# Kernel tuning notes

Measured on AMD Instinct MI355X. Metric: run time of the kernel, lower is better.

The kernel has to match this reference:

```python
import jax, jax.numpy as jnp
import numpy as np

# Model dims (from init_kwargs)
D_MODEL = 1024
D_STATE = 64
D_CONV = 4
EXPAND = 2
HEADDIM = 128
NGROUPS = 1
D_INNER = EXPAND * D_MODEL              # 2048
NHEADS = D_INNER // HEADDIM             # 16
CONV_DIM = D_INNER + 2 * NGROUPS * D_STATE   # 2176
D_IN_PROJ = 2 * D_INNER + 2 * NGROUPS * D_STATE + NHEADS  # 4240
BATCH, SEQLEN = 2, 2048
DT_MIN, DT_MAX, DT_FLOOR = 1e-3, 1e-1, 1e-4
RMS_EPS = 1e-5


def setup_inputs() -> dict:
    key = jax.random.key(0)
    ks = jax.random.split(key, 8)
    u = jax.random.normal(ks[0], (BATCH, SEQLEN, D_MODEL), jnp.float32)
    in_proj_w = jax.random.normal(ks[1], (D_IN_PROJ, D_MODEL), jnp.float32) * 0.02
    conv_w = jax.random.normal(ks[2], (CONV_DIM, 1, D_CONV), jnp.float32) * 0.2
    conv_b = jax.random.normal(ks[3], (CONV_DIM,), jnp.float32) * 0.02
    # dt_bias init: inverse-softplus of dt ~ LogUniform(dt_min, dt_max)
    dt = jnp.exp(jax.random.uniform(ks[4], (NHEADS,)) * (jnp.log(DT_MAX) - jnp.log(DT_MIN)) + jnp.log(DT_MIN))
    dt = jnp.maximum(dt, DT_FLOOR)
    dt_bias = dt + jnp.log(-jnp.expm1(-dt))
    A_log = jnp.log(jax.random.uniform(ks[5], (NHEADS,), minval=1.0, maxval=16.0))
    D_param = jnp.ones((NHEADS,), jnp.float32)
    norm_w = jnp.ones((D_INNER,), jnp.float32)
    out_proj_w = jax.random.normal(ks[6], (D_MODEL, D_INNER), jnp.float32) * 0.02
    return {"u": u, "in_proj_w": in_proj_w, "conv_w": conv_w, "conv_b": conv_b,
            "dt_bias": dt_bias, "A_log": A_log, "D_param": D_param,
            "norm_w": norm_w, "out_proj_w": out_proj_w}


def _mamba2_forward(u, in_proj_w, conv_w, conv_b, dt_bias, A_log, D_param, norm_w, out_proj_w):
    B, L, _ = u.shape
    zxbcdt = jnp.einsum('bld,ed->ble', u, in_proj_w)  # (B, L, D_IN_PROJ)
    z = zxbcdt[..., :D_INNER]
    xBC = zxbcdt[..., D_INNER:D_INNER + CONV_DIM]
    dt = jax.nn.softplus(zxbcdt[..., D_INNER + CONV_DIM:] + dt_bias)  # (B, L, H)

    # Depthwise causal conv1d + SiLU
    xc = jnp.swapaxes(xBC, 1, 2)  # (B, C, L)
    xc = jax.lax.conv_general_dilated(xc, conv_w, window_strides=(1,),
                                      padding=[(D_CONV - 1, 0)],
                                      feature_group_count=CONV_DIM)
    xc = jax.nn.silu(xc + conv_b[None, :, None])
    xBC = jnp.swapaxes(xc, 1, 2)  # (B, L, C)

    x = xBC[..., :D_INNER].reshape(B, L, NHEADS, HEADDIM)
    Bmat = xBC[..., D_INNER:D_INNER + D_STATE]          # (B, L, N), ngroups=1
    Cmat = xBC[..., D_INNER + D_STATE:]                 # (B, L, N)

    A = -jnp.exp(A_log)  # (H,)

    def step(state, inp):
        dt_t, x_t, B_t, C_t = inp  # (B,H), (B,H,P), (B,N), (B,N)
        dA = jnp.exp(dt_t * A)[:, :, None, None]
        state = state * dA + (dt_t[:, :, None, None] * x_t[:, :, :, None]) * B_t[:, None, None, :]
        y_t = jnp.einsum('bhpn,bn->bhp', state, C_t) + D_param[None, :, None] * x_t
        return state, y_t

    state0 = jnp.zeros((B, NHEADS, HEADDIM, D_STATE), u.dtype)
    inputs = (jnp.moveaxis(dt, 1, 0), jnp.moveaxis(x, 1, 0),
              jnp.moveaxis(Bmat, 1, 0), jnp.moveaxis(Cmat, 1, 0))
    _, ys = jax.lax.scan(step, state0, inputs)
    y = jnp.moveaxis(ys, 0, 1).reshape(B, L, D_INNER)

    # RMSNormGated (norm_before_gate=False): gate first, then normalize
    yg = y * jax.nn.silu(z)
    rms = jax.lax.rsqrt(jnp.mean(yg * yg, axis=-1, keepdims=True) + RMS_EPS)
    yn = yg * rms * norm_w

    return jnp.einsum('ble,de->bld', yn, out_proj_w)


def reference(u, in_proj_w, conv_w, conv_b, dt_bias, A_log, D_param, norm_w, out_proj_w):
    return _mamba2_forward(u, in_proj_w, conv_w, conv_b, dt_bias, A_log, D_param, norm_w, out_proj_w)
```

## Files before the change

### kernel.cpp

```cpp
#include <hip/hip_runtime.h>
#include <cstdint>
#include <cstddef>

#define D_MODEL   1024
#define D_STATE   64
#define D_CONV    4
#define HEADDIM   128
#define NHEADS    16
#define D_INNER   2048
#define CONV_DIM  2176
#define D_IN_PROJ 4240
#define NPAD      4352
#define BATCH     2
#define SEQLEN    2048
#define NROWS     (BATCH*SEQLEN)
#define CHUNK     64
#define NCHUNK    (SEQLEN/CHUNK)

using u16   = unsigned short;
using s16x8 = __attribute__((ext_vector_type(8))) short;
using f32x4 = __attribute__((ext_vector_type(4))) float;

__device__ __forceinline__ u16 f2bf(float f) {
    union { float f; unsigned u; } v; v.f = f;
    unsigned r = v.u + 0x7fffu + ((v.u >> 16) & 1u);
    return (u16)(r >> 16);
}
__device__ __forceinline__ float bf2f(u16 x) {
    union { unsigned u; float f; } v; v.u = ((unsigned)x) << 16;
    return v.f;
}

__device__ __forceinline__ void gload16(const u16* g, u16* l) {
    __builtin_amdgcn_global_load_lds(
        (const __attribute__((address_space(1))) unsigned int*)g,
        (__attribute__((address_space(3))) unsigned int*)l, 16, 0, 0);
}

__device__ __forceinline__ void cp8(const float* in, u16* out, int i) {
    const float4* p = (const float4*)(in + (size_t)i * 8);
    float4 a = p[0], b = p[1];
    u16 o[8] = {f2bf(a.x), f2bf(a.y), f2bf(a.z), f2bf(a.w),
                f2bf(b.x), f2bf(b.y), f2bf(b.z), f2bf(b.w)};
    *(uint4*)(out + (size_t)i * 8) = *(const uint4*)o;
}

#define CVT_N0 (NROWS*D_MODEL/8)
#define CVT_N1 (NPAD*128)
#define CVT_N2 (D_MODEL*D_INNER/8)
__global__ __launch_bounds__(256) void cvt_all(
    const float* __restrict__ u, const float* __restrict__ w_in,
    const float* __restrict__ w_out,
    u16* __restrict__ u_bf, u16* __restrict__ w_in_bf, u16* __restrict__ w_out_bf)
{
    int i = blockIdx.x * 256 + threadIdx.x;
    if (i < CVT_N0) {
        cp8(u, u_bf, i);
    } else if (i < CVT_N0 + CVT_N1) {
        int j = i - CVT_N0;
        int row = j >> 7, seg = j & 127;
        u16 o[8] = {0,0,0,0,0,0,0,0};
        if (row < D_IN_PROJ) {
            const float4* p = (const float4*)(w_in + (size_t)row * D_MODEL + seg * 8);
            float4 a = p[0], b = p[1];
            o[0]=f2bf(a.x); o[1]=f2bf(a.y); o[2]=f2bf(a.z); o[3]=f2bf(a.w);
            o[4]=f2bf(b.x); o[5]=f2bf(b.y); o[6]=f2bf(b.z); o[7]=f2bf(b.w);
        }
        *(uint4*)(w_in_bf + (size_t)j * 8) = *(const uint4*)o;
    } else if (i < CVT_N0 + CVT_N1 + CVT_N2) {
        cp8(w_out, w_out_bf, i - CVT_N0 - CVT_N1);
    }
}

#define CPITCH 136
__global__ __launch_bounds__(512) void gemm_in512(
    const u16* __restrict__ A, const u16* __restrict__ B, int K,
    u16* __restrict__ C0, int n1, int ld0,
    u16* __restrict__ C1, int n2, int ld1,
    u16* __restrict__ C2, int n3, int ld2)
{
    __shared__ u16 smem[4 * 128 * 64];

    const int tid  = threadIdx.x;
    const int wid  = tid >> 6;
    const int lane = tid & 63;
    const int wm   = wid >> 2, wn = wid & 3;

    const int gx   = gridDim.x;
    int orig = blockIdx.y * gx + blockIdx.x;
    const int xcd = orig & 7;
    const int loc = orig >> 3;
    const int mt  = (xcd >> 1) * 8  + (loc & 7);
    const int nt  = (xcd & 1) * 17 + (loc >> 3);
    const int m0 = mt * 128, n0 = nt * 128;

    const int lrow = lane >> 3;
    const int lseg = (lane & 7) ^ lrow;
    const u16* gA = A + (size_t)(m0 + lrow) * K + lseg * 8;
    const u16* gB = B + (size_t)(n0 + lrow) * K + lseg * 8;

    f32x4 acc[4][2];
    #pragma unroll
    for (int i = 0; i < 4; ++i)
        #pragma unroll
        for (int j = 0; j < 2; ++j)
            acc[i][j] = (f32x4){0.f, 0.f, 0.f, 0.f};

    const int fr = lane & 15, fq = lane >> 4;
    const int nstep = K >> 6;

    auto stage = [&](int buf, int k0) {
        u16* sAp = smem + buf * 8192;
        u16* sBp = smem + 16384 + buf * 8192;
        #pragma unroll
        for (int i = 0; i < 2; ++i) {
            const int r0 = (i * 8 + wid) * 8;
            gload16(gA + (size_t)r0 * K + k0, sAp + r0 * 64);
            gload16(gB + (size_t)r0 * K + k0, sBp + r0 * 64);
        }
    };

    stage(0, 0);
    int cur = 0;
    for (int step = 0; step < nstep; ++step) {
        if (step + 1 < nstep) {
            stage(cur ^ 1, (step + 1) * 64);
            asm volatile("s_waitcnt vmcnt(4)" ::: "memory");
        } else {
            asm volatile("s_waitcnt vmcnt(0)" ::: "memory");
        }
        __builtin_amdgcn_s_barrier();
        __builtin_amdgcn_sched_barrier(0);

        const u16* sAc = smem + cur * 8192;
        const u16* sBc = smem + 16384 + cur * 8192;
        #pragma unroll
        for (int ks = 0; ks < 2; ++ks) {
            s16x8 bfr[2];
            #pragma unroll
            for (int ni = 0; ni < 2; ++ni) {
                const int row = wn * 32 + ni * 16 + fr;
                const int bo = row * 128 + ((ks * 64 + fq * 16) ^ ((row & 7) << 4));
                bfr[ni] = *(const s16x8*)((const char*)sBc + bo);
            }
            #pragma unroll
            for (int mi = 0; mi < 4; ++mi) {
                const int row = wm * 64 + mi * 16 + fr;
                const int bo = row * 128 + ((ks * 64 + fq * 16) ^ ((row & 7) << 4));
                s16x8 af = *(const s16x8*)((const char*)sAc + bo);
                #pragma unroll
                for (int ni = 0; ni < 2; ++ni)
                    acc[mi][ni] = __builtin_amdgcn_mfma_f32_16x16x32_bf16(
                        af, bfr[ni], acc[mi][ni], 0, 0, 0);
            }
        }

        __builtin_amdgcn_sched_barrier(0);
        __builtin_amdgcn_s_barrier();
        cur ^= 1;
    }
    __builtin_amdgcn_sched_barrier(0);

    u16* sC = smem;
    #pragma unroll
    for (int mi = 0; mi < 4; ++mi) {
        #pragma unroll
        for (int j = 0; j < 4; ++j) {
            const int rl = wm * 64 + mi * 16 + fq * 4 + j;
            #pragma unroll
            for (int ni = 0; ni < 2; ++ni) {
                const int cl = wn * 32 + ni * 16 + fr;
                sC[rl * CPITCH + cl] = f2bf(acc[mi][ni][j]);
            }
        }
    }
    __syncthreads();
    #pragma unroll
    for (int k2 = 0; k2 < 4; ++k2) {
        const int g  = tid + k2 * 512;
        const int rl = g >> 4, cg = g & 15;
        uint4 v = *(const uint4*)&sC[rl * CPITCH + cg * 8];
        const int r = m0 + rl, c = n0 + cg * 8;
        if (c < n1)      *(uint4*)(C0 + (size_t)r * ld0 + c)        = v;
        else if (c < n2) *(uint4*)(C1 + (size_t)r * ld1 + (c - n1)) = v;
        else if (c < n3) *(uint4*)(C2 + (size_t)r * ld2 + (c - n2)) = v;
    }
}

__global__ __launch_bounds__(512) void gemm_out512(
    const u16* __restrict__ A, const u16* __restrict__ B, int K,
    float* __restrict__ C, int N)
{
    __shared__ u16 smem[4 * 128 * 64];

    const int tid  = threadIdx.x;
    const int wid  = tid >> 6;
    const int lane = tid & 63;
    const int wm   = wid >> 2, wn = wid & 3;

    const int gx   = gridDim.x;
    const int nwg  = gx * gridDim.y;
    const int cpx  = nwg >> 3;
    int orig = blockIdx.y * gx + blockIdx.x;
    int wg   = (orig & 7) * cpx + (orig >> 3);
    const int m0 = (wg / gx) * 128, n0 = (wg % gx) * 128;

    const int lrow = lane >> 3;
    const int lseg = (lane & 7) ^ lrow;
    const u16* gA = A + (size_t)(m0 + lrow) * K + lseg * 8;
    const u16* gB = B + (size_t)(n0 + lrow) * K + lseg * 8;

    f32x4 acc[4][2];
    #pragma unroll
    for (int i = 0; i < 4; ++i)
        #pragma unroll
        for (int j = 0; j < 2; ++j)
            acc[i][j] = (f32x4){0.f, 0.f, 0.f, 0.f};

    const int fr = lane & 15, fq = lane >> 4;
    const int nstep = K >> 6;

    auto stage = [&](int buf, int k0) {
        u16* sAp = smem + buf * 8192;
        u16* sBp = smem + 16384 + buf * 8192;
        #pragma unroll
        for (int i = 0; i < 2; ++i) {
            const int r0 = (i * 8 + wid) * 8;
            gload16(gA + (size_t)r0 * K + k0, sAp + r0 * 64);
            gload16(gB + (size_t)r0 * K + k0, sBp + r0 * 64);
        }
    };

    stage(0, 0);
    int cur = 0;
    for (int step = 0; step < nstep; ++step) {
        if (step + 1 < nstep) {
            stage(cur ^ 1, (step + 1) * 64);
            asm volatile("s_waitcnt vmcnt(4)" ::: "memory");
        } else {
            asm volatile("s_waitcnt vmcnt(0)" ::: "memory");
        }
        __builtin_amdgcn_s_barrier();
        __builtin_amdgcn_sched_barrier(0);

        const u16* sAc = smem + cur * 8192;
        const u16* sBc = smem + 16384 + cur * 8192;
        #pragma unroll
        for (int ks = 0; ks < 2; ++ks) {
            s16x8 bfr[2];
            #pragma unroll
            for (int ni = 0; ni < 2; ++ni) {
                const int row = wn * 32 + ni * 16 + fr;
                const int bo = row * 128 + ((ks * 64 + fq * 16) ^ ((row & 7) << 4));
                bfr[ni] = *(const s16x8*)((const char*)sBc + bo);
            }
            #pragma unroll
            for (int mi = 0; mi < 4; ++mi) {
                const int row = wm * 64 + mi * 16 + fr;
                const int bo = row * 128 + ((ks * 64 + fq * 16) ^ ((row & 7) << 4));
                s16x8 af = *(const s16x8*)((const char*)sAc + bo);
                #pragma unroll
                for (int ni = 0; ni < 2; ++ni)
                    acc[mi][ni] = __builtin_amdgcn_mfma_f32_16x16x32_bf16(
                        af, bfr[ni], acc[mi][ni], 0, 0, 0);
            }
        }

        __builtin_amdgcn_sched_barrier(0);
        __builtin_amdgcn_s_barrier();
        cur ^= 1;
    }
    __builtin_amdgcn_sched_barrier(0);

    float* sCf = (float*)smem;
    #pragma unroll
    for (int h2 = 0; h2 < 2; ++h2) {
        if (wm == h2) {
            #pragma unroll
            for (int mi = 0; mi < 4; ++mi)
                #pragma unroll
                for (int j = 0; j < 4; ++j) {
                    const int rl = mi * 16 + fq * 4 + j;
                    #pragma unroll
                    for (int ni = 0; ni < 2; ++ni) {
                        const int cl = wn * 32 + ni * 16 + fr;
                        sCf[rl * 132 + cl] = acc[mi][ni][j];
                    }
                }
        }
        __syncthreads();
        #pragma unroll
        for (int k2 = 0; k2 < 4; ++k2) {
            const int g  = tid + k2 * 512;
            const int rl = g >> 5, cg = g & 31;
            float4 v = *(const float4*)&sCf[rl * 132 + cg * 4];
            *(float4*)(C + (size_t)(m0 + h2 * 64 + rl) * N + n0 + cg * 4) = v;
        }
        __syncthreads();
    }
}

#define NCONV8 (NROWS*(CONV_DIM/8))
__global__ __launch_bounds__(256) void conv_silu_dt(
    const u16* __restrict__ xBC, const float* __restrict__ conv_w,
    const float* __restrict__ conv_b, u16* __restrict__ xconv,
    const u16* __restrict__ dtraw, const float* __restrict__ dt_bias,
    float* __restrict__ dtw)
{
    int idx = blockIdx.x * 256 + threadIdx.x;
    if (idx < NCONV8) {
        int c8  = idx % (CONV_DIM / 8);
        int row = idx / (CONV_DIM / 8);
        int l   = row % SEQLEN;
        int b   = row / SEQLEN;
        int c0  = c8 * 8;
        const u16* src = xBC + (size_t)(b * SEQLEN) * CONV_DIM + c0;

        uint4 z4 = {0u, 0u, 0u, 0u};
        uint4 v3 = *(const uint4*)(src + (size_t)l * CONV_DIM);
        uint4 v2 = (l >= 1) ? *(const uint4*)(src + (size_t)(l-1) * CONV_DIM) : z4;
        uint4 v1 = (l >= 2) ? *(const uint4*)(src + (size_t)(l-2) * CONV_DIM) : z4;
        uint4 v0 = (l >= 3) ? *(const uint4*)(src + (size_t)(l-3) * CONV_DIM) : z4;
        const u16* p0 = (const u16*)&v0; const u16* p1 = (const u16*)&v1;
        const u16* p2 = (const u16*)&v2; const u16* p3 = (const u16*)&v3;

        u16 o[8];
        #pragma unroll
        for (int j = 0; j < 8; ++j) {
            const float4 w4 = *(const float4*)(conv_w + (size_t)(c0 + j) * 4);
            float acc = conv_b[c0 + j]
                      + bf2f(p0[j]) * w4.x + bf2f(p1[j]) * w4.y
                      + bf2f(p2[j]) * w4.z + bf2f(p3[j]) * w4.w;
            o[j] = f2bf(acc / (1.f + expf(-acc)));
        }
        *(uint4*)(xconv + (size_t)row * CONV_DIM + c0) = *(const uint4*)o;
    } else {
        int k = idx - NCONV8;
        if (k < NROWS * NHEADS) {
            int h = k & (NHEADS - 1);
            float v = bf2f(dtraw[k]) + dt_bias[h];
            dtw[k] = (v > 20.f) ? v : log1pf(expf(v));
        }
    }
}

__global__ __launch_bounds__(256) void chunk_state(
    const u16* __restrict__ xconv, const float* __restrict__ dtw,
    const float* __restrict__ A_log, u16* __restrict__ Sbuf,
    float* __restrict__ Tbuf)
{
    const int blk = blockIdx.x;
    const int k  = blk & (NCHUNK-1);
    const int bh = blk >> 5;
    const int b  = bh >> 4, h = bh & 15;
    const int tid = threadIdx.x;
    const int wid = tid >> 6, lane = tid & 63;
    const float A = -expf(A_log[h]);

    __shared__ u16 arena[12288];
    u16* sWBT = arena;
    u16* sXT  = arena + 4096;
    u16* eT   = arena;
    float* sdt = (float*)arena;
    float* sW  = sdt + CHUNK;

    const int t0 = k * CHUNK;
    const u16* xc = xconv + (size_t)(b*SEQLEN + t0) * CONV_DIM;

    if (tid < CHUNK)
        sdt[tid] = dtw[(size_t)(b*SEQLEN + t0 + tid)*NHEADS + h];
    __syncthreads();
    if (tid < CHUNK) {
        float a = 0.f, pref = 0.f;
        for (int r = 0; r < CHUNK; ++r) {
            a += sdt[r] * A;
            if (r == tid) pref = a;
        }
        sW[tid] = __expf(a - pref) * sdt[tid];
        if (tid == 0) Tbuf[bh*NCHUNK + k] = a;
    }
    __syncthreads();

    const int s_stg = tid >> 2;
    const float wv = sW[s_stg];
    __syncthreads();

    {
        const int nb = tid & 3;
        uint4 b0 = *(const uint4*)(xc + (size_t)s_stg*CONV_DIM + D_INNER + nb*16);
        uint4 b1 = *(const uint4*)(xc + (size_t)s_stg*CONV_DIM + D_INNER + nb*16 + 8);
        const u16* pb0 = (const u16*)&b0; const u16* pb1 = (const u16*)&b1;
        const int cb = s_stg * 2, cbase = (cb & ~15), coff = (cb & 15);
        #pragma unroll
        for (int j = 0; j < 16; ++j) {
            const int n = nb * 16 + j;
            const u16 val = f2bf(wv * bf2f(j < 8 ? pb0[j] : pb1[j - 8]));
            const int bo = n * 128 + (cbase ^ ((n & 7) << 4)) + coff;
            *(u16*)((char*)sWBT + bo) = val;
        }
    }
    {
        const int pg = tid & 3;
        const int cb = s_stg * 2, cbase = (cb & ~15), coff = (cb & 15);
        #pragma unroll
        for (int i = 0; i < 4; ++i) {
            const int pb = pg * 32 + i * 8;
            uint4 xv = *(const uint4*)(xc + (size_t)s_stg*CONV_DIM + h*HEADDIM + pb);
            const u16* xp = (const u16*)&xv;
            #pragma unroll
            for (int j = 0; j < 8; ++j) {
                const int p = pb + j;
                const int bo = p * 128 + (cbase ^ ((p & 7) << 4)) + coff;
                *(u16*)((char*)sXT + bo) = xp[j];
            }
        }
    }
    __syncthreads();

    const int fr = lane & 15, fq = lane >> 4;
    f32x4 accS[8];
    #pragma unroll
    for (int i = 0; i < 8; ++i) accS[i] = (f32x4){0.f, 0.f, 0.f, 0.f};

    #pragma unroll
    for (int ks = 0; ks < 2; ++ks) {
        const int nrow = wid * 16 + fr;
        const int boA = nrow * 128 + ((ks * 64 + fq * 16) ^ ((nrow & 7) << 4));
        s16x8 afr = *(const s16x8*)((const char*)sWBT + boA);
        #pragma unroll
        for (int pt = 0; pt < 8; ++pt) {
            const int p = pt * 16 + fr;
            const int boB = p * 128 + ((ks * 64 + fq * 16) ^ ((p & 7) << 4));
            s16x8 bfrB = *(const s16x8*)((const char*)sXT + boB);
            accS[pt] = __builtin_amdgcn_mfma_f32_16x16x32_bf16(afr, bfrB, accS[pt], 0, 0, 0);
        }
    }
    __syncthreads();

    #pragma unroll
    for (int pt = 0; pt < 8; ++pt) {
        #pragma unroll
        for (int r = 0; r < 4; ++r) {
            const int n = wid * 16 + fq * 4 + r;
            eT[n * CPITCH + pt * 16 + fr] = f2bf(accS[pt][r]);
        }
    }
    __syncthreads();
    u16* So = Sbuf + ((size_t)bh*NCHUNK + k)*(D_STATE*HEADDIM);
    #pragma unroll
    for (int k2 = 0; k2 < 4; ++k2) {
        const int g  = tid + k2 * 256;
        const int rl = g >> 4, cg = g & 15;
        uint4 v = *(const uint4*)&eT[rl * CPITCH + cg * 8];
        *(uint4*)(So + (size_t)rl * HEADDIM + cg * 8) = v;
    }
}

__global__ __launch_bounds__(256) void chunk_seq_par(u16* __restrict__ Sbuf,
                                                     const float* __restrict__ Tbuf)
{
    const int blk = blockIdx.x;
    const int bh  = blk >> 3;
    const int sub = blk & 7;
    __shared__ float seT[NCHUNK];
    if (threadIdx.x < NCHUNK)
        seT[threadIdx.x] = __expf(Tbuf[bh*NCHUNK + threadIdx.x]);
    __syncthreads();

    const int idx4 = sub * 256 + threadIdx.x;
    u16* base = Sbuf + (size_t)bh*NCHUNK*(D_STATE*HEADDIM) + (size_t)idx4*4;
    float run[4];
    #pragma unroll
    for (int j = 0; j < 4; ++j) run[j] = 0.f;
    for (int k = 0; k < NCHUNK; ++k) {
        u16* p = base + (size_t)k * (D_STATE*HEADDIM);
        uint2 v = *(const uint2*)p;
        const u16* pv = (const u16*)&v;
        const float eT = seT[k];
        u16 o[4];
        #pragma unroll
        for (int j = 0; j < 4; ++j) {
            float tmp = bf2f(pv[j]);
            o[j] = f2bf(run[j]);
            run[j] = run[j] * eT + tmp;
        }
        *(uint2*)p = *(const uint2*)o;
    }
}

__global__ __launch_bounds__(256) void chunk_output(
    const u16* __restrict__ xconv, const float* __restrict__ dtw,
    const float* __restrict__ A_log, const float* __restrict__ D_param,
    const u16* __restrict__ Sbuf, u16* __restrict__ y)
{
    const int blk = blockIdx.x;
    const int k  = blk & (NCHUNK-1);
    const int bh = blk >> 5;
    const int b  = bh >> 4, h = bh & 15;
    const int tid = threadIdx.x;
    const int wid = tid >> 6, lane = tid & 63;
    const float A  = -expf(A_log[h]);
    const float Dp = D_param[h];

    __shared__ u16 arena[3 * 8192];
    u16* Mfull = arena;
    u16* sXT   = arena + 8192;
    u16* sST   = arena + 16384;
    u16* eT    = arena + 8192;
    float* sdt = (float*)Mfull;
    float* sL  = sdt + CHUNK;

    const int t0 = k * CHUNK;
    const u16* xc = xconv + (size_t)(b*SEQLEN + t0) * CONV_DIM;
    const u16* Sinit = Sbuf + ((size_t)bh*NCHUNK + k)*(D_STATE*HEADDIM);

    if (tid < CHUNK)
        sdt[tid] = dtw[(size_t)(b*SEQLEN + t0 + tid)*NHEADS + h];
    __syncthreads();
    if (tid < CHUNK) {
        float a = 0.f, pref = 0.f;
        for (int r = 0; r < CHUNK; ++r) {
            a += sdt[r] * A;
            if (r == tid) pref = a;
        }
        sL[tid] = pref;
    }
    __syncthreads();

    const int fr = lane & 15, fq = lane >> 4;
    float4 sL4 = *(const float4*)&sL[wid * 16 + fq * 4];
    const float Lt[4] = {sL4.x, sL4.y, sL4.z, sL4.w};
    float pre_L[4], pre_dt[4];
    #pragma unroll
    for (int sf = 0; sf < 4; ++sf) {
        const int s_row = sf * 16 + fr;
        pre_L[sf]  = sL[s_row];
        pre_dt[sf] = sdt[s_row];
    }
    const int tM = tid >> 2, nbM = tid & 3;
    const float elM = __expf(sL[tM]);
    __syncthreads();

    {
        const int sr = tid >> 2;
        const int pg = tid & 3;
        #pragma unroll
        for (int i = 0; i < 4; ++i) {
            const int pb = pg * 32 + i * 8;
            uint4 xv = *(const uint4*)(xc + (size_t)sr * CONV_DIM + h * HEADDIM + pb);
            const u16* xp = (const u16*)&xv;
            uint4 sv = *(const uint4*)(Sinit + (size_t)sr * HEADDIM + pb);
            const u16* sp = (const u16*)&sv;
            const int cb = sr * 2;
            const int cbase = (cb & ~15), coff = (cb & 15);
            #pragma unroll
            for (int j = 0; j < 8; ++j) {
                const int p = pb + j;
                const int bo = p * 128 + (cbase ^ ((p & 7) << 4)) + coff;
                *(u16*)((char*)sXT + bo) = xp[j];
                *(u16*)((char*)sST + bo) = sp[j];
            }
        }
    }

    {
        const int t_row = wid * 16 + fr;
        s16x8 cfrag[2];
        #pragma unroll
        for (int ks = 0; ks < 2; ++ks)
            cfrag[ks] = *(const s16x8*)(xc + (size_t)t_row*CONV_DIM + D_INNER + D_STATE
                                        + ks*32 + fq*8);

        #pragma unroll
        for (int sf = 0; sf < 4; ++sf) {
            const int s_row = sf * 16 + fr;
            f32x4 g = (f32x4){0.f, 0.f, 0.f, 0.f};
            #pragma unroll
            for (int ks = 0; ks < 2; ++ks) {
                s16x8 bfrag = *(const s16x8*)(xc + (size_t)s_row*CONV_DIM + D_INNER
                                              + ks*32 + fq*8);
                g = __builtin_amdgcn_mfma_f32_16x16x32_bf16(cfrag[ks], bfrag, g, 0, 0, 0);
            }
            const float Ls  = pre_L[sf];
            const float dts = pre_dt[sf];
            const int cb = s_row * 2;
            const int cbase = (cb & ~15), coff = (cb & 15);
            #pragma unroll
            for (int r = 0; r < 4; ++r) {
                const int t = wid * 16 + fq * 4 + r;
                const float e = __expf(fminf(Lt[r] - Ls, 0.f)) * dts;
                const float val = (s_row <= t) ? g[r] * e : 0.f;
                const int bo = t * 256 + (cbase ^ ((t & 7) << 4)) + coff;
                *(u16*)((char*)Mfull + bo) = f2bf(val);
            }
        }
    }
    {
        uint4 c0 = *(const uint4*)(xc + (size_t)tM*CONV_DIM + D_INNER + D_STATE + nbM*16);
        uint4 c1 = *(const uint4*)(xc + (size_t)tM*CONV_DIM + D_INNER + D_STATE + nbM*16 + 8);
        const u16* pc0 = (const u16*)&c0; const u16* pc1 = (const u16*)&c1;
        u16 o[16];
        #pragma unroll
        for (int j = 0; j < 16; ++j)
            o[j] = f2bf(elM * bf2f(j < 8 ? pc0[j] : pc1[j - 8]));
        #pragma unroll
        for (int u2 = 0; u2 < 2; ++u2) {
            const int cb = 128 + nbM * 32 + u2 * 16;
            const int bo = tM * 256 + (cb ^ ((tM & 7) << 4));
            *(uint4*)((char*)Mfull + bo) = *(const uint4*)&o[u2 * 8];
        }
    }
    __syncthreads();

    f32x4 accB[8];
    #pragma unroll
    for (int i = 0; i < 8; ++i) accB[i] = (f32x4){0.f, 0.f, 0.f, 0.f};

    #pragma unroll
    for (int ks = 0; ks < 4; ++ks) {
        const int ta = wid * 16 + fr;
        const int boA = ta * 256 + ((ks * 64 + fq * 16) ^ ((ta & 7) << 4));
        s16x8 afr = *(const s16x8*)((const char*)Mfull + boA);
        const u16* src = (ks < 2) ? sXT : sST;
        const int cbB = (ks & 1) * 64 + fq * 16;
        #pragma unroll
        for (int pt = 0; pt < 8; ++pt) {
            const int p = pt * 16 + fr;
            const int boB = p * 128 + (cbB ^ ((p & 7) << 4));
            s16x8 bfrB = *(const s16x8*)((const char*)src + boB);
            accB[pt] = __builtin_amdgcn_mfma_f32_16x16x32_bf16(afr, bfrB, accB[pt], 0, 0, 0);
        }
    }

    #pragma unroll
    for (int pt = 0; pt < 8; ++pt) {
        const int p = pt * 16 + fr;
        #pragma unroll
        for (int r = 0; r < 4; ++r) {
            const int t = wid * 16 + fq * 4 + r;
            const int cb = t * 2;
            const int bo = p * 128 + ((cb & ~15) ^ ((p & 7) << 4)) + (cb & 15);
            accB[pt][r] += Dp * bf2f(*(const u16*)((const char*)sXT + bo));
        }
    }
    __syncthreads();

    #pragma unroll
    for (int pt = 0; pt < 8; ++pt) {
        #pragma unroll
        for (int r = 0; r < 4; ++r) {
            const int t = wid * 16 + fq * 4 + r;
            eT[t * CPITCH + pt * 16 + fr] = f2bf(accB[pt][r]);
        }
    }
    __syncthreads();
    #pragma unroll
    for (int k2 = 0; k2 < 4; ++k2) {
        const int g  = tid + k2 * 256;
        const int rl = g >> 4, cg = g & 15;
        uint4 v = *(const uint4*)&eT[rl * CPITCH + cg * 8];
        *(uint4*)(y + ((size_t)(b*SEQLEN + t0 + rl))*D_INNER + h*HEADDIM + cg*8) = v;
    }
}

__global__ __launch_bounds__(256) void gate_rmsnorm(const u16* __restrict__ z,
                                                    const u16* __restrict__ y,
                                                    const float* __restrict__ norm_w,
                                                    u16* __restrict__ yn)
{
    const int row = blockIdx.x;
    const int tid = threadIdx.x;
    const u16* zr = z + (size_t)row * D_INNER + tid * 8;
    const u16* yr = y + (size_t)row * D_INNER + tid * 8;
    u16*       o  = yn + (size_t)row * D_INNER + tid * 8;

    uint4 zv4 = *(const uint4*)zr;
    uint4 yv4 = *(const uint4*)yr;
    const u16* zp = (const u16*)&zv4;
    const u16* yp = (const u16*)&yv4;

    float vals[8];
    float ss = 0.f;
    #pragma unroll
    for (int j = 0; j < 8; ++j) {
        float zv = bf2f(zp[j]);
        float g  = bf2f(yp[j]) * (zv / (1.f + expf(-zv)));
        vals[j] = g;
        ss += g * g;
    }
    #pragma unroll
    for (int off = 32; off > 0; off >>= 1) ss += __shfl_down(ss, off);
    __shared__ float red[4];
    __shared__ float sscale;
    int wid = tid >> 6, lane = tid & 63;
    if (lane == 0) red[wid] = ss;
    __syncthreads();
    if (tid == 0)
        sscale = rsqrtf((red[0]+red[1]+red[2]+red[3]) / (float)D_INNER + 1e-5f);
    __syncthreads();
    float rms = sscale;
    const float4* nw = (const float4*)(norm_w + tid * 8);
    float4 w0 = nw[0], w1 = nw[1];
    float wv[8] = {w0.x,w0.y,w0.z,w0.w,w1.x,w1.y,w1.z,w1.w};
    u16 ov[8];
    #pragma unroll
    for (int j = 0; j < 8; ++j) ov[j] = f2bf(vals[j] * rms * wv[j]);
    *(uint4*)o = *(const uint4*)ov;
}

extern "C" void kernel_launch(void* const* d_in, const int* in_sizes, int n_in,
                              void* d_out, int out_size, void* d_ws, size_t ws_size,
                              hipStream_t stream)
{
    const float* u          = (const float*)d_in[0];
    const float* in_proj_w  = (const float*)d_in[1];
    const float* conv_w     = (const float*)d_in[2];
    const float* conv_b     = (const float*)d_in[3];
    const float* dt_bias    = (const float*)d_in[4];
    const float* A_log      = (const float*)d_in[5];
    const float* D_param    = (const float*)d_in[6];
    const float* norm_w     = (const float*)d_in[7];
    const float* out_proj_w = (const float*)d_in[8];
    float* out = (float*)d_out;

    char* w = (char*)d_ws;
    u16* z_bf     = (u16*)w;  w += (size_t)NROWS * D_INNER  * 2;
    u16* xBC_bf   = (u16*)w;  w += (size_t)NROWS * CONV_DIM * 2;
    u16* xconv_bf = (u16*)w;  w += (size_t)NROWS * CONV_DIM * 2;
    u16* yb_bf    = (u16*)w;  w += (size_t)NROWS * D_INNER  * 2;
    u16* dtraw_bf = (u16*)w;  w += (size_t)NROWS * NHEADS   * 2;
    float* dtw    = (float*)w; w += (size_t)NROWS * NHEADS  * 4;
    float* Tbuf   = (float*)w; w += (size_t)BATCH*NHEADS*NCHUNK * 4;
    u16* Sbuf     = (u16*)w;  w += (size_t)BATCH*NHEADS*NCHUNK*D_STATE*HEADDIM * 2;
    u16* u_bf     = (u16*)w;  w += (size_t)NROWS * D_MODEL  * 2;
    u16* w_in_bf  = (u16*)w;  w += (size_t)NPAD  * D_MODEL  * 2;
    u16* w_out_bf = (u16*)w;  w += (size_t)D_MODEL * D_INNER * 2;
    u16* yn_bf    = xconv_bf;

    cvt_all<<<(CVT_N0+CVT_N1+CVT_N2 + 255)/256, 256, 0, stream>>>(
        u, in_proj_w, out_proj_w, u_bf, w_in_bf, w_out_bf);

    dim3 g1(NPAD/128, NROWS/128);
    gemm_in512<<<g1, 512, 0, stream>>>(u_bf, w_in_bf, D_MODEL,
                                       z_bf, D_INNER, D_INNER,
                                       xBC_bf, D_INNER + CONV_DIM, CONV_DIM,
                                       dtraw_bf, D_IN_PROJ, NHEADS);

    int ntot = NCONV8 + NROWS * NHEADS;
    conv_silu_dt<<<(ntot + 255) / 256, 256, 0, stream>>>(
        xBC_bf, conv_w, conv_b, xconv_bf, dtraw_bf, dt_bias, dtw);

    chunk_state<<<BATCH*NHEADS*NCHUNK, 256, 0, stream>>>(xconv_bf, dtw, A_log, Sbuf, Tbuf);
    chunk_seq_par<<<BATCH*NHEADS*8, 256, 0, stream>>>(Sbuf, Tbuf);
    chunk_output<<<BATCH*NHEADS*NCHUNK, 256, 0, stream>>>(xconv_bf, dtw, A_log, D_param,
                                                          Sbuf, yb_bf);

    gate_rmsnorm<<<NROWS, 256, 0, stream>>>(z_bf, yb_bf, norm_w, yn_bf);

    dim3 g6(D_MODEL/128, NROWS/128);
    gemm_out512<<<g6, 512, 0, stream>>>(yn_bf, w_out_bf, D_INNER, out, D_MODEL);
}
```

Baseline: 170.5 us.

## Shrink chunk_output LDS by time-sharing X and S tiles in one buffer

Reduces the shared memory footprint of chunk_output from three 16KB regions to two. The intra-chunk M matrix and the state-extension matrix are stored as separate halves, and the X^T and S^T tiles share one buffer that is reloaded between the two MFMA phases. The output transpose is staged in two 32-row halves so it fits in the shared region. The aim is more resident blocks per CU, at the cost of additional barriers and a serialized state load after the first GEMM.

```diff
diff --git a/kernel.cpp b/kernel.cpp
--- a/kernel.cpp
+++ b/kernel.cpp
@@ -502,12 +502,11 @@
     const float A  = -expf(A_log[h]);
     const float Dp = D_param[h];
 
-    __shared__ u16 arena[3 * 8192];
-    u16* Mfull = arena;
-    u16* sXT   = arena + 8192;
-    u16* sST   = arena + 16384;
-    u16* eT    = arena + 8192;
-    float* sdt = (float*)Mfull;
+    __shared__ u16 arena[16384];
+    u16* Ms   = arena;
+    u16* Mext = arena + 4096;
+    u16* sT   = arena + 8192;
+    float* sdt = (float*)arena;
     float* sL  = sdt + CHUNK;
 
     const int t0 = k * CHUNK;
@@ -542,23 +541,19 @@
     __syncthreads();
 
     {
-        const int sr = tid >> 2;
-        const int pg = tid & 3;
+        const int sr = tM;
+        const int pg = nbM;
+        const int cb = sr * 2, cbase = (cb & ~15), coff = (cb & 15);
         #pragma unroll
         for (int i = 0; i < 4; ++i) {
             const int pb = pg * 32 + i * 8;
             uint4 xv = *(const uint4*)(xc + (size_t)sr * CONV_DIM + h * HEADDIM + pb);
             const u16* xp = (const u16*)&xv;
-            uint4 sv = *(const uint4*)(Sinit + (size_t)sr * HEADDIM + pb);
-            const u16* sp = (const u16*)&sv;
-            const int cb = sr * 2;
-            const int cbase = (cb & ~15), coff = (cb & 15);
             #pragma unroll
             for (int j = 0; j < 8; ++j) {
                 const int p = pb + j;
                 const int bo = p * 128 + (cbase ^ ((p & 7) << 4)) + coff;
-                *(u16*)((char*)sXT + bo) = xp[j];
-                *(u16*)((char*)sST + bo) = sp[j];
+                *(u16*)((char*)sT + bo) = xp[j];
             }
         }
     }
@@ -590,8 +585,8 @@
                 const int t = wid * 16 + fq * 4 + r;
                 const float e = __expf(fminf(Lt[r] - Ls, 0.f)) * dts;
                 const float val = (s_row <= t) ? g[r] * e : 0.f;
-                const int bo = t * 256 + (cbase ^ ((t & 7) << 4)) + coff;
-                *(u16*)((char*)Mfull + bo) = f2bf(val);
+                const int bo = t * 128 + (cbase ^ ((t & 7) << 4)) + coff;
+                *(u16*)((char*)Ms + bo) = f2bf(val);
             }
         }
     }
@@ -605,9 +600,9 @@
             o[j] = f2bf(elM * bf2f(j < 8 ? pc0[j] : pc1[j - 8]));
         #pragma unroll
         for (int u2 = 0; u2 < 2; ++u2) {
-            const int cb = 128 + nbM * 32 + u2 * 16;
-            const int bo = tM * 256 + (cb ^ ((tM & 7) << 4));
-            *(uint4*)((char*)Mfull + bo) = *(const uint4*)&o[u2 * 8];
+            const int cb = nbM * 32 + u2 * 16;
+            const int bo = tM * 128 + (cb ^ ((tM & 7) << 4));
+            *(uint4*)((char*)Mext + bo) = *(const uint4*)&o[u2 * 8];
         }
     }
     __syncthreads();
@@ -617,21 +612,18 @@
     for (int i = 0; i < 8; ++i) accB[i] = (f32x4){0.f, 0.f, 0.f, 0.f};
 
     #pragma unroll
-    for (int ks = 0; ks < 4; ++ks) {
+    for (int ks = 0; ks < 2; ++ks) {
         const int ta = wid * 16 + fr;
-        const int boA = ta * 256 + ((ks * 64 + fq * 16) ^ ((ta & 7) << 4));
-        s16x8 afr = *(const s16x8*)((const char*)Mfull + boA);
-        const u16* src = (ks < 2) ? sXT : sST;
-        const int cbB = (ks & 1) * 64 + fq * 16;
+        const int boA = ta * 128 + ((ks * 64 + fq * 16) ^ ((ta & 7) << 4));
+        s16x8 afr = *(const s16x8*)((const char*)Ms + boA);
         #pragma unroll
         for (int pt = 0; pt < 8; ++pt) {
             const int p = pt * 16 + fr;
-            const int boB = p * 128 + (cbB ^ ((p & 7) << 4));
-            s16x8 bfrB = *(const s16x8*)((const char*)src + boB);
+            const int boB = p * 128 + ((ks * 64 + fq * 16) ^ ((p & 7) << 4));
+            s16x8 bfrB = *(const s16x8*)((const char*)sT + boB);
             accB[pt] = __builtin_amdgcn_mfma_f32_16x16x32_bf16(afr, bfrB, accB[pt], 0, 0, 0);
         }
     }
-
     #pragma unroll
     for (int pt = 0; pt < 8; ++pt) {
         const int p = pt * 16 + fr;
@@ -640,26 +632,69 @@
             const int t = wid * 16 + fq * 4 + r;
             const int cb = t * 2;
             const int bo = p * 128 + ((cb & ~15) ^ ((p & 7) << 4)) + (cb & 15);
-            accB[pt][r] += Dp * bf2f(*(const u16*)((const char*)sXT + bo));
-        }
-    }
-    __syncthreads();
-
-    #pragma unroll
-    for (int pt = 0; pt < 8; ++pt) {
-        #pragma unroll
-        for (int r = 0; r < 4; ++r) {
-            const int t = wid * 16 + fq * 4 + r;
-            eT[t * CPITCH + pt * 16 + fr] = f2bf(accB[pt][r]);
-        }
-    }
-    __syncthreads();
-    #pragma unroll
-    for (int k2 = 0; k2 < 4; ++k2) {
-        const int g  = tid + k2 * 256;
-        const int rl = g >> 4, cg = g & 15;
-        uint4 v = *(const uint4*)&eT[rl * CPITCH + cg * 8];
-        *(uint4*)(y + ((size_t)(b*SEQLEN + t0 + rl))*D_INNER + h*HEADDIM + cg*8) = v;
+            accB[pt][r] += Dp * bf2f(*(const u16*)((const char*)sT + bo));
+        }
+    }
+    __syncthreads();
+
+    {
+        const int sr = tM;
+        const int pg = nbM;
+        const int cb = sr * 2, cbase = (cb & ~15), coff = (cb & 15);
+        #pragma unroll
+        for (int i = 0; i < 4; ++i) {
+            const int pb = pg * 32 + i * 8;
+            uint4 sv = *(const uint4*)(Sinit + (size_t)sr * HEADDIM + pb);
+            const u16* sp = (const u16*)&sv;
+            #pragma unroll
+            for (int j = 0; j < 8; ++j) {
+                const int p = pb + j;
+                const int bo = p * 128 + (cbase ^ ((p & 7) << 4)) + coff;
+                *(u16*)((char*)sT + bo) = sp[j];
+            }
+        }
+    }
+    __syncthreads();
+
+    #pragma unroll
+    for (int ks = 0; ks < 2; ++ks) {
+        const int ta = wid * 16 + fr;
+        const int boA = ta * 128 + ((ks * 64 + fq * 16) ^ ((ta & 7) << 4));
+        s16x8 afr = *(const s16x8*)((const char*)Mext + boA);
+        #pragma unroll
+        for (int pt = 0; pt < 8; ++pt) {
+            const int p = pt * 16 + fr;
+            const int boB = p * 128 + ((ks * 64 + fq * 16) ^ ((p & 7) << 4));
+            s16x8 bfrB = *(const s16x8*)((const char*)sT + boB);
+            accB[pt] = __builtin_amdgcn_mfma_f32_16x16x32_bf16(afr, bfrB, accB[pt], 0, 0, 0);
+        }
+    }
+    __syncthreads();
+
+    u16* eT = sT;
+    #pragma unroll
+    for (int hh = 0; hh < 2; ++hh) {
+        if ((wid >> 1) == hh) {
+            #pragma unroll
+            for (int pt = 0; pt < 8; ++pt) {
+                #pragma unroll
+                for (int r = 0; r < 4; ++r) {
+                    const int t  = wid * 16 + fq * 4 + r;
+                    const int rl = t & 31;
+                    eT[rl * CPITCH + pt * 16 + fr] = f2bf(accB[pt][r]);
+                }
+            }
+        }
+        __syncthreads();
+        #pragma unroll
+        for (int k2 = 0; k2 < 2; ++k2) {
+            const int g  = tid + k2 * 256;
+            const int rl = g >> 4, cg = g & 15;
+            uint4 v = *(const uint4*)&eT[rl * CPITCH + cg * 8];
+            *(uint4*)(y + ((size_t)(b*SEQLEN + t0 + hh*32 + rl))*D_INNER
+                      + h*HEADDIM + cg*8) = v;
+        }
+        __syncthreads();
     }
 }
 
```

Result: no change. 170.6 us (+0.0%).
